# Performance work log

Hardware: AMD Instinct MI355X
Metric: run time of the kernel (lower is better)

## Reference

```python
import jax, jax.numpy as jnp
import numpy as np

N, E, IN_F, EDGE_F, HID, S = 200000, 600000, 28, 4, 128, 20000
NUM_LAYERS = 4
L = NUM_LAYERS - 1
BN_EPS = 1e-5


def setup_inputs() -> dict:
    key = jax.random.key(0)
    ks = jax.random.split(key, 20)
    p = lambda k, shape: (jax.random.normal(k, shape, dtype=jnp.float32) * 0.1)
    return {
        'x': jax.random.normal(ks[0], (N, IN_F), dtype=jnp.float32),
        'edge_index': jax.random.randint(ks[1], (2, E), 0, N),
        'edge_attr': jax.random.normal(ks[2], (E, EDGE_F), dtype=jnp.float32),
        'edge_weight': jax.random.uniform(ks[3], (E,), dtype=jnp.float32),
        'node_mask': (jax.random.uniform(ks[4], (N,)) > 0.5).astype(jnp.float32),
        'subgraphs2nodes': jax.random.randint(ks[5], (N,), 0, S),
        # layer-1 params (in_features -> hidden)
        'be1_W1': p(ks[6], (EDGE_F, IN_F)), 'be1_b1': jnp.zeros((IN_F,), jnp.float32),
        'be1_W2': p(ks[7], (IN_F, IN_F)), 'be1_b2': jnp.zeros((IN_F,), jnp.float32),
        'm1_W1': p(ks[8], (IN_F, HID)), 'm1_b1': jnp.zeros((HID,), jnp.float32),
        'm1_W2': p(ks[9], (HID, HID)), 'm1_b2': jnp.zeros((HID,), jnp.float32),
        'bn1_g': jnp.ones((HID,), jnp.float32), 'bn1_b': jnp.zeros((HID,), jnp.float32),
        'eps1': jnp.zeros((), jnp.float32),
        # layers 2..NUM_LAYERS, stacked (hidden -> hidden)
        'beW1': p(ks[10], (L, EDGE_F, HID)), 'beb1': jnp.zeros((L, HID), jnp.float32),
        'beW2': p(ks[11], (L, HID, HID)), 'beb2': jnp.zeros((L, HID), jnp.float32),
        'mW1': p(ks[12], (L, HID, HID)), 'mb1': jnp.zeros((L, HID), jnp.float32),
        'mW2': p(ks[13], (L, HID, HID)), 'mb2': jnp.zeros((L, HID), jnp.float32),
        'bng': jnp.ones((L, HID), jnp.float32), 'bnb': jnp.zeros((L, HID), jnp.float32),
        'eps': jnp.zeros((L,), jnp.float32),
    }


def _mlp2(h, W1, b1, W2, b2):
    # Linear -> ReLU -> Linear
    return jnp.dot(jax.nn.relu(jnp.dot(h, W1) + b1), W2) + b2


def _gine(x, src, dst, edge_attr, edge_weight, eps,
          beW1, beb1, beW2, beb2, W1, b1, W2, b2, g, beta):
    # bond encoder on edge features
    e = _mlp2(edge_attr, beW1, beb1, beW2, beb2)            # [E, d]
    # message: relu(x_j + e_ij) * w_ij, aggregated at dst via scatter-add
    m = jax.nn.relu(x[src] + e) * edge_weight[:, None]      # [E, d]
    aggr = jax.ops.segment_sum(m, dst, num_segments=N)      # [N, d]
    h = (1.0 + eps) * x + aggr
    # node MLP: Linear,ReLU,Linear,BN(train mode),ReLU
    h = _mlp2(h, W1, b1, W2, b2)
    mu = jnp.mean(h, axis=0)
    var = jnp.mean((h - mu) ** 2, axis=0)
    h = (h - mu) * jax.lax.rsqrt(var + BN_EPS) * g + beta
    return jax.nn.relu(h)


def reference(x, edge_index, edge_attr, edge_weight, node_mask, subgraphs2nodes,
              be1_W1, be1_b1, be1_W2, be1_b2, m1_W1, m1_b1, m1_W2, m1_b2,
              bn1_g, bn1_b, eps1,
              beW1, beb1, beW2, beb2, mW1, mb1, mW2, mb2, bng, bnb, eps):
    src, dst = edge_index[0], edge_index[1]
    h = _gine(x, src, dst, edge_attr, edge_weight, eps1,
              be1_W1, be1_b1, be1_W2, be1_b2,
              m1_W1, m1_b1, m1_W2, m1_b2, bn1_g, bn1_b)
    for i in range(L):
        h_new = _gine(h, src, dst, edge_attr, edge_weight, eps[i],
                      beW1[i], beb1[i], beW2[i], beb2[i],
                      mW1[i], mb1[i], mW2[i], mb2[i], bng[i], bnb[i])
        h = h + h_new  # residual
    # float node_mask branch + global_add_pool over subgraphs2nodes
    h = h * node_mask[:, None]
    return jax.ops.segment_sum(h, subgraphs2nodes, num_segments=S)  # [S, HID]
```

## Files before the change

kernel.cpp:

```cpp
#include <hip/hip_runtime.h>
#include <hip/hip_bf16.h>


#define BNEPS 1e-5f
#define LDA 136
#define SCAN_NB 240

typedef __attribute__((ext_vector_type(8))) short bf16x8;
typedef __attribute__((ext_vector_type(8))) unsigned short u16x8;
typedef __attribute__((ext_vector_type(4))) float f32x4;

__device__ inline short f2bf(float f) {
    __hip_bfloat16 h = __float2bfloat16(f);
    return *reinterpret_cast<short*>(&h);
}
__device__ inline unsigned short f2bfu(float f) {
    __hip_bfloat16 h = __float2bfloat16(f);
    return *reinterpret_cast<unsigned short*>(&h);
}
__device__ inline float bf2f(unsigned short u) {
    union { unsigned int i; float f; } v; v.i = ((unsigned int)u) << 16; return v.f;
}


__global__ __launch_bounds__(256) void k_prep(
    const float* __restrict__ m1W2, const float* __restrict__ beW2,
    const float* __restrict__ mW1, const float* __restrict__ mW2,
    const float* __restrict__ m1W1, const float* __restrict__ be1W2,
    short* __restrict__ out, short* __restrict__ out1, short* __restrict__ out28)
{
    __shared__ float tileS[64][65];
    int b = blockIdx.x;
    if (b == 40) {
        for (int i = threadIdx.x; i < 4096; i += 256) {
            int j = i & 7, sub = (i >> 3) & 63, nt = i >> 9;
            int quad = sub >> 4, l15 = sub & 15;
            int n = nt * 16 + l15, k = quad * 8 + j;
            out1[i] = (k < 28) ? f2bf(m1W1[(size_t)k * 128 + n]) : (short)0;
        }
        return;
    }
    if (b == 41) {
        for (int i = threadIdx.x; i < 1024; i += 256) {
            int j = i & 7, lane = (i >> 3) & 63, nt = i >> 9;
            int quad = lane >> 4, l15 = lane & 15;
            int n = nt * 16 + l15, k = quad * 8 + j;
            out28[i] = (n < 28 && k < 28) ? f2bf(be1W2[(size_t)k * 28 + n]) : (short)0;
        }
        return;
    }
    int mat = b >> 2, t = b & 3;
    const float* Wsrc;
    if (mat == 0) Wsrc = m1W2;
    else {
        int l = (mat - 1) / 3, which = (mat - 1) % 3;
        Wsrc = (which == 0) ? beW2 + (size_t)l * 16384
             : (which == 1) ? mW1 + (size_t)l * 16384
             :                mW2 + (size_t)l * 16384;
    }
    short* dst = out + (size_t)mat * 16384;
    int tr = (t >> 1) * 64, tc = (t & 1) * 64;
    for (int i = threadIdx.x; i < 4096; i += 256) {
        int r = i >> 6, c = i & 63;
        tileS[r][c] = Wsrc[(size_t)(tr + r) * 128 + (tc + c)];
    }
    __syncthreads();
    for (int i = threadIdx.x; i < 4096; i += 256) {
        int kl = i & 63, nl = i >> 6;
        int n = tc + nl, k = tr + kl;
        int fo = (((n >> 4) * 4 + (k >> 5)) * 64 + (((k >> 3) & 3) * 16 + (n & 15))) * 8 + (k & 7);
        dst[fo] = f2bf(tileS[kl][nl]);
    }
}

__global__ __launch_bounds__(256) void k_prepx(
    const float* __restrict__ x, unsigned short* __restrict__ xbf, int N)
{
    int total = N * 32;
    for (int i = blockIdx.x * 256 + threadIdx.x; i < total; i += gridDim.x * 256) {
        int n = i >> 5, c = i & 31;
        xbf[i] = (c < 28) ? f2bfu(x[(size_t)n * 28 + c]) : (unsigned short)0;
    }
}

__global__ __launch_bounds__(256) void k_count(
    const int* __restrict__ ei, int* __restrict__ counts, int E)
{
    for (int e = blockIdx.x * 256 + threadIdx.x; e < E; e += gridDim.x * 256)
        atomicAdd(&counts[ei[E + e]], 1);
}

__global__ __launch_bounds__(256) void k_count2(
    const int* __restrict__ s2n, const float* __restrict__ mask,
    int* __restrict__ counts2, int N)
{
    for (int n = blockIdx.x * 256 + threadIdx.x; n < N; n += gridDim.x * 256)
        if (mask[n] != 0.f) atomicAdd(&counts2[s2n[n]], 1);
}

__global__ __launch_bounds__(256) void k_scanA(
    const int* __restrict__ counts, int* __restrict__ bsum, int N, int seg)
{
    __shared__ int red[256];
    int b = blockIdx.x;
    int lo = b * seg, hi = min(lo + seg, N);
    int s = 0;
    for (int i = lo + threadIdx.x; i < hi; i += 256) s += counts[i];
    red[threadIdx.x] = s;
    __syncthreads();
    for (int d = 128; d > 0; d >>= 1) {
        if (threadIdx.x < d) red[threadIdx.x] += red[threadIdx.x + d];
        __syncthreads();
    }
    if (threadIdx.x == 0) bsum[b] = red[0];
}

__global__ __launch_bounds__(256) void k_scanB(
    int* __restrict__ bsum, int nb, int* __restrict__ offs, int N)
{
    __shared__ int sh[256];
    int v = (threadIdx.x < nb) ? bsum[threadIdx.x] : 0;
    sh[threadIdx.x] = v;
    __syncthreads();
    for (int d = 1; d < 256; d <<= 1) {
        int t = (threadIdx.x >= d) ? sh[threadIdx.x - d] : 0;
        __syncthreads();
        sh[threadIdx.x] += t;
        __syncthreads();
    }
    if (threadIdx.x < nb) bsum[threadIdx.x] = sh[threadIdx.x] - v;
    if (threadIdx.x == 0) offs[N] = sh[255];
}

__global__ __launch_bounds__(256) void k_scanC(
    const int* __restrict__ counts, const int* __restrict__ bsum,
    int* __restrict__ offs, int* __restrict__ cursor, int N, int seg)
{
    __shared__ int sh[256];
    int b = blockIdx.x;
    int lo = b * seg, hi = min(lo + seg, N);
    int base = bsum[b];
    for (int t0 = lo; t0 < hi; t0 += 256) {
        int i = t0 + threadIdx.x;
        int v = (i < hi) ? counts[i] : 0;
        sh[threadIdx.x] = v;
        __syncthreads();
        for (int d = 1; d < 256; d <<= 1) {
            int t = (threadIdx.x >= d) ? sh[threadIdx.x - d] : 0;
            __syncthreads();
            sh[threadIdx.x] += t;
            __syncthreads();
        }
        int excl = base + sh[threadIdx.x] - v;
        if (i < hi) { offs[i] = excl; cursor[i] = excl; }
        int tileTotal = sh[255];
        __syncthreads();
        base += tileTotal;
    }
}

__global__ __launch_bounds__(256) void k_scatter(
    const int* __restrict__ ei, const float* __restrict__ ew,
    const float4* __restrict__ ea4,
    int* __restrict__ cursor, int2* __restrict__ pmeta,
    float4* __restrict__ pea4, int E)
{
    for (int e = blockIdx.x * 256 + threadIdx.x; e < E; e += gridDim.x * 256) {
        int d = ei[E + e];
        int pos = atomicAdd(&cursor[d], 1);
        pmeta[pos] = make_int2(ei[e], __float_as_int(ew[e]));
        pea4[pos] = ea4[e];
    }
}

__global__ __launch_bounds__(256) void k_scatter2(
    const int* __restrict__ s2n, const float* __restrict__ mask,
    int* __restrict__ cursor2, int* __restrict__ perm2, int N)
{
    for (int n = blockIdx.x * 256 + threadIdx.x; n < N; n += gridDim.x * 256)
        if (mask[n] != 0.f) {
            int pos = atomicAdd(&cursor2[s2n[n]], 1);
            perm2[pos] = n;
        }
}

__global__ __launch_bounds__(256, 3) void k_emsg(
    const float4* __restrict__ pea4,
    const float* __restrict__ W1, const float* __restrict__ b1,
    const short* __restrict__ W2f, const float* __restrict__ b2,
    unsigned short* __restrict__ emsg, const int* __restrict__ offs,
    int n0, int n1)
{
    __shared__ short As[64 * LDA];
    __shared__ short Bs[16384];
    int e0 = offs[n0], e1 = offs[n1];
    int tid = threadIdx.x;
    int w = tid >> 6, lane = tid & 63;
    int l15 = lane & 15, quad = lane >> 4;
    int rb = w * 16;
    for (int i = tid; i < 2048; i += 256)
        *(bf16x8*)&Bs[i * 8] = *(const bf16x8*)&W2f[i * 8];
    int c2 = lane * 2;
    float w1a[4], w1b[4];
    #pragma unroll
    for (int a = 0; a < 4; ++a) { w1a[a] = W1[a * 128 + c2]; w1b[a] = W1[a * 128 + c2 + 1]; }
    float b1a = b1[c2], b1b = b1[c2 + 1];
    float b2r[8];
    #pragma unroll
    for (int nt = 0; nt < 8; ++nt) b2r[nt] = b2[nt * 16 + l15];
    __syncthreads();

    const float* peaf = (const float*)pea4;
    int numTiles = (e1 - e0 + 63) >> 6;
    for (int tile = blockIdx.x; tile < numTiles; tile += gridDim.x) {
        int base = e0 + tile * 64;
        int eidx = base + rb + (lane >> 2);
        float v = (eidx < e1) ? peaf[(size_t)(base + rb) * 4 + lane] : 0.f;
        #pragma unroll
        for (int e = 0; e < 16; ++e) {
            float a0v = __shfl(v, e * 4 + 0);
            float a1v = __shfl(v, e * 4 + 1);
            float a2v = __shfl(v, e * 4 + 2);
            float a3v = __shfl(v, e * 4 + 3);
            float t0 = fmaf(a0v, w1a[0], fmaf(a1v, w1a[1], fmaf(a2v, w1a[2], fmaf(a3v, w1a[3], b1a))));
            float t1 = fmaf(a0v, w1b[0], fmaf(a1v, w1b[1], fmaf(a2v, w1b[2], fmaf(a3v, w1b[3], b1b))));
            unsigned int pk = ((unsigned int)f2bfu(fmaxf(t1, 0.f)) << 16) | f2bfu(fmaxf(t0, 0.f));
            *(unsigned int*)&As[(rb + e) * LDA + c2] = pk;
        }
        f32x4 acc[8];
        #pragma unroll
        for (int nt = 0; nt < 8; ++nt) acc[nt] = (f32x4){0.f, 0.f, 0.f, 0.f};
        #pragma unroll
        for (int kt = 0; kt < 4; ++kt) {
            bf16x8 af = *(bf16x8*)&As[(rb + l15) * LDA + kt * 32 + quad * 8];
            #pragma unroll
            for (int nt = 0; nt < 8; ++nt) {
                bf16x8 bf = *(const bf16x8*)&Bs[((nt * 4 + kt) * 64 + lane) * 8];
                acc[nt] = __builtin_amdgcn_mfma_f32_16x16x32_bf16(af, bf, acc[nt], 0, 0, 0);
            }
        }
        #pragma unroll
        for (int nt = 0; nt < 8; ++nt) {
            #pragma unroll
            for (int r = 0; r < 4; ++r)
                As[(rb + quad * 4 + r) * LDA + nt * 16 + l15] = f2bf(acc[nt][r] + b2r[nt]);
        }
        #pragma unroll
        for (int it = 0; it < 4; ++it) {
            int arow = rb + it * 4 + quad;
            int gr = base + arow;
            if (gr < e1)
                *(bf16x8*)&emsg[(size_t)(gr - e0) * 128 + l15 * 8] = *(bf16x8*)&As[arow * LDA + l15 * 8];
        }
    }
}

__global__ __launch_bounds__(256, 4) void k_emsg28_mm(
    const float4* __restrict__ pea4,
    const float* __restrict__ W1, const float* __restrict__ b1,
    const short* __restrict__ W2f28,
    const float* __restrict__ b2,
    unsigned short* __restrict__ emsg28, int E)
{
    __shared__ short As[64 * 40];
    int tid = threadIdx.x;
    int w = tid >> 6, lane = tid & 63;
    int l15 = lane & 15, quad = lane >> 4;
    int rb = w * 16;
    bf16x8 B0 = *(const bf16x8*)&W2f28[(size_t)lane * 8];
    bf16x8 B1 = *(const bf16x8*)&W2f28[(size_t)(64 + lane) * 8];
    int c2 = l15 * 2;
    bool act = (c2 < 28);
    float w1a[4], w1b[4], b1a, b1b;
    #pragma unroll
    for (int a = 0; a < 4; ++a) {
        w1a[a] = act ? W1[a * 28 + c2] : 0.f;
        w1b[a] = act ? W1[a * 28 + c2 + 1] : 0.f;
    }
    b1a = act ? b1[c2] : 0.f;
    b1b = act ? b1[c2 + 1] : 0.f;
    float b2r0 = b2[l15];
    float b2r1 = (l15 < 12) ? b2[16 + l15] : 0.f;

    const float* peaf = (const float*)pea4;
    int numTiles = (E + 63) >> 6;
    for (int tile = blockIdx.x; tile < numTiles; tile += gridDim.x) {
        int base = tile * 64;
        int eidx = base + rb + (lane >> 2);
        float v = (eidx < E) ? peaf[(size_t)(base + rb) * 4 + lane] : 0.f;
        #pragma unroll
        for (int e = 0; e < 16; ++e) {
            float a0v = __shfl(v, e * 4 + 0);
            float a1v = __shfl(v, e * 4 + 1);
            float a2v = __shfl(v, e * 4 + 2);
            float a3v = __shfl(v, e * 4 + 3);
            float t0 = fmaf(a0v, w1a[0], fmaf(a1v, w1a[1], fmaf(a2v, w1a[2], fmaf(a3v, w1a[3], b1a))));
            float t1 = fmaf(a0v, w1b[0], fmaf(a1v, w1b[1], fmaf(a2v, w1b[2], fmaf(a3v, w1b[3], b1b))));
            unsigned int pk = ((unsigned int)f2bfu(fmaxf(t1, 0.f)) << 16) | f2bfu(fmaxf(t0, 0.f));
            if (quad == (e & 3))
                *(unsigned int*)&As[(rb + e) * 40 + c2] = pk;
        }
        f32x4 acc0 = (f32x4){0.f, 0.f, 0.f, 0.f};
        f32x4 acc1 = (f32x4){0.f, 0.f, 0.f, 0.f};
        bf16x8 af = *(bf16x8*)&As[(rb + l15) * 40 + quad * 8];
        acc0 = __builtin_amdgcn_mfma_f32_16x16x32_bf16(af, B0, acc0, 0, 0, 0);
        acc1 = __builtin_amdgcn_mfma_f32_16x16x32_bf16(af, B1, acc1, 0, 0, 0);
        #pragma unroll
        for (int r = 0; r < 4; ++r) {
            As[(rb + quad * 4 + r) * 40 + l15] = f2bf(acc0[r] + b2r0);
            As[(rb + quad * 4 + r) * 40 + 16 + l15] = f2bf(acc1[r] + b2r1);
        }
        #pragma unroll
        for (int it = 0; it < 4; ++it) {
            int arow = rb + it * 4 + quad;
            int gr = base + arow;
            if (gr < E && l15 < 14)
                *(ushort2*)&emsg28[(size_t)gr * 28 + c2] = *(ushort2*)&As[arow * 40 + c2];
        }
    }
}

__global__ __launch_bounds__(256) void k_gather(
    const unsigned short* __restrict__ h, const int* __restrict__ offs,
    const int2* __restrict__ pmeta, const unsigned short* __restrict__ emsg,
    unsigned short* __restrict__ a0,
    const float* __restrict__ epsp, int epsIdx,
    int n0, int n1)
{
    int grp = threadIdx.x >> 5, lane = threadIdx.x & 31;
    int n = n0 + blockIdx.x * 8 + grp;
    if (n >= n1) return;
    int e0 = offs[n0];
    int k0 = offs[n], k1 = offs[n + 1];
    float s = 1.0f + epsp[epsIdx];
    ushort4 hv0 = *(const ushort4*)&h[(size_t)n * 128 + lane * 4];
    float m0 = s * bf2f(hv0.x), m1 = s * bf2f(hv0.y);
    float m2 = s * bf2f(hv0.z), m3 = s * bf2f(hv0.w);
    int2 mtA, mtB;
    ushort4 evA, hvA, evB, hvB;
    if (k0 < k1) {
        mtA = pmeta[k0];
        evA = *(const ushort4*)&emsg[(size_t)(k0 - e0) * 128 + lane * 4];
        hvA = *(const ushort4*)&h[(size_t)mtA.x * 128 + lane * 4];
    }
    if (k0 + 1 < k1) {
        mtB = pmeta[k0 + 1];
        evB = *(const ushort4*)&emsg[(size_t)(k0 + 1 - e0) * 128 + lane * 4];
        hvB = *(const ushort4*)&h[(size_t)mtB.x * 128 + lane * 4];
    }
    for (int k = k0; k < k1; ++k) {
        float w = __int_as_float(mtA.y);
        m0 += fmaxf(bf2f(hvA.x) + bf2f(evA.x), 0.f) * w;
        m1 += fmaxf(bf2f(hvA.y) + bf2f(evA.y), 0.f) * w;
        m2 += fmaxf(bf2f(hvA.z) + bf2f(evA.z), 0.f) * w;
        m3 += fmaxf(bf2f(hvA.w) + bf2f(evA.w), 0.f) * w;
        mtA = mtB; evA = evB; hvA = hvB;
        if (k + 2 < k1) {
            mtB = pmeta[k + 2];
            evB = *(const ushort4*)&emsg[(size_t)(k + 2 - e0) * 128 + lane * 4];
            hvB = *(const ushort4*)&h[(size_t)mtB.x * 128 + lane * 4];
        }
    }
    ushort4 o;
    o.x = f2bfu(m0); o.y = f2bfu(m1); o.z = f2bfu(m2); o.w = f2bfu(m3);
    *(ushort4*)&a0[(size_t)n * 128 + lane * 4] = o;
}

__global__ __launch_bounds__(256) void k_gather28(
    const float* __restrict__ x, const unsigned short* __restrict__ xbf,
    const int* __restrict__ offs,
    const int2* __restrict__ pmeta, const unsigned short* __restrict__ emsg28,
    const float* __restrict__ eps1, float* __restrict__ u28, int N)
{
    int grp = threadIdx.x >> 5, lane = threadIdx.x & 31;
    int n = blockIdx.x * 8 + grp;
    if (n >= N || lane >= 28) return;
    float s = 1.0f + eps1[0];
    int k0 = offs[n], k1 = offs[n + 1];
    float m = 0.f;
    int2 mtA, mtB;
    unsigned short eA = 0, xA = 0, eB = 0, xB = 0;
    if (k0 < k1) {
        mtA = pmeta[k0];
        eA = emsg28[(size_t)k0 * 28 + lane];
        xA = xbf[(size_t)mtA.x * 32 + lane];
    }
    if (k0 + 1 < k1) {
        mtB = pmeta[k0 + 1];
        eB = emsg28[(size_t)(k0 + 1) * 28 + lane];
        xB = xbf[(size_t)mtB.x * 32 + lane];
    }
    for (int k = k0; k < k1; ++k) {
        float w = __int_as_float(mtA.y);
        m += fmaxf(bf2f(xA) + bf2f(eA), 0.f) * w;
        mtA = mtB; eA = eB; xA = xB;
        if (k + 2 < k1) {
            mtB = pmeta[k + 2];
            eB = emsg28[(size_t)(k + 2) * 28 + lane];
            xB = xbf[(size_t)mtB.x * 32 + lane];
        }
    }
    u28[(size_t)n * 28 + lane] = fmaf(s, x[(size_t)n * 28 + lane], m);
}

__global__ __launch_bounds__(1024, 4) void k_mlp(
    const unsigned short* __restrict__ src, const short* __restrict__ W1f,
    const float* __restrict__ b1, const short* __restrict__ W2f,
    const float* __restrict__ b2, unsigned short* __restrict__ dst,
    float* __restrict__ stats, int N)
{
    __shared__ short Bs1[16384];
    __shared__ short Bs2[16384];
    __shared__ short As[16 * 16 * LDA];
    __shared__ float sstat[256];
    int tid = threadIdx.x;
    for (int i = tid; i < 2048; i += 1024) {
        *(bf16x8*)&Bs1[i * 8] = *(const bf16x8*)&W1f[i * 8];
        *(bf16x8*)&Bs2[i * 8] = *(const bf16x8*)&W2f[i * 8];
    }
    if (tid < 256) sstat[tid] = 0.f;
    int w = tid >> 6, lane = tid & 63;
    int l15 = lane & 15, quad = lane >> 4;
    short* myAs = &As[w * 16 * LDA];
    float b1r[8], b2r[8], lsum[8], lsq[8];
    #pragma unroll
    for (int nt = 0; nt < 8; ++nt) {
        b1r[nt] = b1[nt * 16 + l15]; b2r[nt] = b2[nt * 16 + l15];
        lsum[nt] = 0.f; lsq[nt] = 0.f;
    }
    __syncthreads();

    int numTiles = (N + 255) >> 8;
    for (int tile = blockIdx.x; tile < numTiles; tile += gridDim.x) {
        int rowbase = tile * 256 + w * 16;
        int arow = rowbase + l15;
        const unsigned short* srow = src + (size_t)arow * 128;
        f32x4 acc[8];
        #pragma unroll
        for (int nt = 0; nt < 8; ++nt) acc[nt] = (f32x4){0.f, 0.f, 0.f, 0.f};
        #pragma unroll
        for (int kt = 0; kt < 4; ++kt) {
            bf16x8 af = (arow < N) ? *(const bf16x8*)&srow[kt * 32 + quad * 8]
                                   : (bf16x8){0, 0, 0, 0, 0, 0, 0, 0};
            #pragma unroll
            for (int nt = 0; nt < 8; ++nt) {
                bf16x8 bf = *(const bf16x8*)&Bs1[((nt * 4 + kt) * 64 + lane) * 8];
                acc[nt] = __builtin_amdgcn_mfma_f32_16x16x32_bf16(af, bf, acc[nt], 0, 0, 0);
            }
        }
        #pragma unroll
        for (int nt = 0; nt < 8; ++nt)
            #pragma unroll
            for (int r = 0; r < 4; ++r)
                myAs[(quad * 4 + r) * LDA + nt * 16 + l15] =
                    f2bf(fmaxf(acc[nt][r] + b1r[nt], 0.f));
        #pragma unroll
        for (int nt = 0; nt < 8; ++nt) acc[nt] = (f32x4){0.f, 0.f, 0.f, 0.f};
        #pragma unroll
        for (int kt = 0; kt < 4; ++kt) {
            bf16x8 af = *(bf16x8*)&myAs[l15 * LDA + kt * 32 + quad * 8];
            #pragma unroll
            for (int nt = 0; nt < 8; ++nt) {
                bf16x8 bf = *(const bf16x8*)&Bs2[((nt * 4 + kt) * 64 + lane) * 8];
                acc[nt] = __builtin_amdgcn_mfma_f32_16x16x32_bf16(af, bf, acc[nt], 0, 0, 0);
            }
        }
        #pragma unroll
        for (int nt = 0; nt < 8; ++nt) {
            int row0 = rowbase + quad * 4;
            #pragma unroll
            for (int r = 0; r < 4; ++r) {
                float z = acc[nt][r] + b2r[nt];
                if (row0 + r < N) { lsum[nt] += z; lsq[nt] = fmaf(z, z, lsq[nt]); }
                myAs[(quad * 4 + r) * LDA + nt * 16 + l15] = f2bf(z);
            }
        }
        #pragma unroll
        for (int s = 0; s < 4; ++s) {
            int i = lane + s * 64;
            int lrow = i >> 4, c8 = i & 15;
            int rr = rowbase + lrow;
            if (rr < N)
                *(bf16x8*)&dst[(size_t)rr * 128 + c8 * 8] = *(bf16x8*)&myAs[lrow * LDA + c8 * 8];
        }
    }
    #pragma unroll
    for (int nt = 0; nt < 8; ++nt) {
        atomicAdd(&sstat[nt * 16 + l15], lsum[nt]);
        atomicAdd(&sstat[128 + nt * 16 + l15], lsq[nt]);
    }
    __syncthreads();
    if (tid < 256) atomicAdd(&stats[tid], sstat[tid]);
}

__global__ __launch_bounds__(1024, 4) void k_mlp1(
    const float* __restrict__ u28, const short* __restrict__ W1f,
    const float* __restrict__ b1, const short* __restrict__ W2f,
    const float* __restrict__ b2, unsigned short* __restrict__ dst,
    float* __restrict__ stats, int N)
{
    __shared__ short Bs1[4096];
    __shared__ short Bs2[16384];
    __shared__ short As[16 * 16 * LDA];
    __shared__ float sstat[256];
    int tid = threadIdx.x;
    if (tid < 512)
        *(bf16x8*)&Bs1[tid * 8] = *(const bf16x8*)&W1f[tid * 8];
    for (int i = tid; i < 2048; i += 1024)
        *(bf16x8*)&Bs2[i * 8] = *(const bf16x8*)&W2f[i * 8];
    if (tid < 256) sstat[tid] = 0.f;
    int w = tid >> 6, lane = tid & 63;
    int l15 = lane & 15, quad = lane >> 4;
    short* myAs = &As[w * 16 * LDA];
    float b1r[8], b2r[8], lsum[8], lsq[8];
    #pragma unroll
    for (int nt = 0; nt < 8; ++nt) {
        b1r[nt] = b1[nt * 16 + l15]; b2r[nt] = b2[nt * 16 + l15];
        lsum[nt] = 0.f; lsq[nt] = 0.f;
    }
    __syncthreads();

    int numTiles = (N + 255) >> 8;
    for (int tile = blockIdx.x; tile < numTiles; tile += gridDim.x) {
        int rowbase = tile * 256 + w * 16;
        int arow = rowbase + l15;
        const float* urow = u28 + (size_t)arow * 28;
        float4 fa = make_float4(0.f, 0.f, 0.f, 0.f);
        float4 fb = make_float4(0.f, 0.f, 0.f, 0.f);
        if (arow < N) {
            fa = *(const float4*)&urow[quad * 8];
            if (quad < 3) fb = *(const float4*)&urow[quad * 8 + 4];
        }
        bf16x8 af1;
        af1[0] = f2bf(fa.x); af1[1] = f2bf(fa.y); af1[2] = f2bf(fa.z); af1[3] = f2bf(fa.w);
        af1[4] = f2bf(fb.x); af1[5] = f2bf(fb.y); af1[6] = f2bf(fb.z); af1[7] = f2bf(fb.w);
        f32x4 acc[8];
        #pragma unroll
        for (int nt = 0; nt < 8; ++nt) acc[nt] = (f32x4){0.f, 0.f, 0.f, 0.f};
        #pragma unroll
        for (int nt = 0; nt < 8; ++nt) {
            bf16x8 bf = *(const bf16x8*)&Bs1[(nt * 64 + lane) * 8];
            acc[nt] = __builtin_amdgcn_mfma_f32_16x16x32_bf16(af1, bf, acc[nt], 0, 0, 0);
        }
        #pragma unroll
        for (int nt = 0; nt < 8; ++nt)
            #pragma unroll
            for (int r = 0; r < 4; ++r)
                myAs[(quad * 4 + r) * LDA + nt * 16 + l15] =
                    f2bf(fmaxf(acc[nt][r] + b1r[nt], 0.f));
        #pragma unroll
        for (int nt = 0; nt < 8; ++nt) acc[nt] = (f32x4){0.f, 0.f, 0.f, 0.f};
        #pragma unroll
        for (int kt = 0; kt < 4; ++kt) {
            bf16x8 af = *(bf16x8*)&myAs[l15 * LDA + kt * 32 + quad * 8];
            #pragma unroll
            for (int nt = 0; nt < 8; ++nt) {
                bf16x8 bf = *(const bf16x8*)&Bs2[((nt * 4 + kt) * 64 + lane) * 8];
                acc[nt] = __builtin_amdgcn_mfma_f32_16x16x32_bf16(af, bf, acc[nt], 0, 0, 0);
            }
        }
        #pragma unroll
        for (int nt = 0; nt < 8; ++nt) {
            int row0 = rowbase + quad * 4;
            #pragma unroll
            for (int r = 0; r < 4; ++r) {
                float z = acc[nt][r] + b2r[nt];
                if (row0 + r < N) { lsum[nt] += z; lsq[nt] = fmaf(z, z, lsq[nt]); }
                myAs[(quad * 4 + r) * LDA + nt * 16 + l15] = f2bf(z);
            }
        }
        #pragma unroll
        for (int s = 0; s < 4; ++s) {
            int i = lane + s * 64;
            int lrow = i >> 4, c8 = i & 15;
            int rr = rowbase + lrow;
            if (rr < N)
                *(bf16x8*)&dst[(size_t)rr * 128 + c8 * 8] = *(bf16x8*)&myAs[lrow * LDA + c8 * 8];
        }
    }
    #pragma unroll
    for (int nt = 0; nt < 8; ++nt) {
        atomicAdd(&sstat[nt * 16 + l15], lsum[nt]);
        atomicAdd(&sstat[128 + nt * 16 + l15], lsq[nt]);
    }
    __syncthreads();
    if (tid < 256) atomicAdd(&stats[tid], sstat[tid]);
}

__global__ __launch_bounds__(128) void k_stats(
    const float* __restrict__ stats, const float* __restrict__ g,
    const float* __restrict__ b, float* __restrict__ ss, float invN)
{
    int j = threadIdx.x;
    float mu  = stats[j] * invN;
    float var = fmaf(stats[128 + j], invN, -mu * mu);
    float sc  = rsqrtf(fmaxf(var, 0.f) + BNEPS) * g[j];
    ss[j] = sc;
    ss[128 + j] = fmaf(-mu, sc, b[j]);
}

__global__ __launch_bounds__(256) void k_bn(
    const unsigned short* __restrict__ z, const float* __restrict__ ss,
    unsigned short* __restrict__ h, int residual, int N)
{
    int idx8 = blockIdx.x * 256 + threadIdx.x;
    int stride = gridDim.x * 256;
    int c0 = (idx8 & 15) * 8;
    float scl[8], sht[8];
    #pragma unroll
    for (int r = 0; r < 8; ++r) { scl[r] = ss[c0 + r]; sht[r] = ss[128 + c0 + r]; }
    int total8 = N * 16;
    for (; idx8 < total8; idx8 += stride) {
        int n = idx8 >> 4;
        u16x8 z8 = *(const u16x8*)&z[(size_t)n * 128 + c0];
        float hn[8];
        #pragma unroll
        for (int r = 0; r < 8; ++r)
            hn[r] = fmaxf(fmaf(bf2f(z8[r]), scl[r], sht[r]), 0.f);
        if (residual) {
            u16x8 h8 = *(const u16x8*)&h[(size_t)n * 128 + c0];
            #pragma unroll
            for (int r = 0; r < 8; ++r) hn[r] += bf2f(h8[r]);
        }
        u16x8 o;
        #pragma unroll
        for (int r = 0; r < 8; ++r) o[r] = f2bfu(hn[r]);
        *(u16x8*)&h[(size_t)n * 128 + c0] = o;
    }
}

__global__ __launch_bounds__(256) void k_poolbn(
    const unsigned short* __restrict__ z, const unsigned short* __restrict__ hprev,
    const float* __restrict__ ss, const int* __restrict__ offs2,
    const int* __restrict__ perm2, float* __restrict__ out, int S)
{
    int w = threadIdx.x >> 6, lane = threadIdx.x & 63;
    int s = blockIdx.x * 4 + w;
    if (s >= S) return;
    int c0 = lane * 2;
    float scl0 = ss[c0], scl1 = ss[c0 + 1];
    float sht0 = ss[128 + c0], sht1 = ss[128 + c0 + 1];
    int k0 = offs2[s], k1 = offs2[s + 1];
    float a0 = 0.f, a1 = 0.f;
    for (int k = k0; k < k1; ++k) {
        int n = perm2[k];
        ushort2 zv = *(const ushort2*)&z[(size_t)n * 128 + c0];
        ushort2 hv = *(const ushort2*)&hprev[(size_t)n * 128 + c0];
        a0 += fmaxf(fmaf(bf2f(zv.x), scl0, sht0), 0.f) + bf2f(hv.x);
        a1 += fmaxf(fmaf(bf2f(zv.y), scl1, sht1), 0.f) + bf2f(hv.y);
    }
    *(float2*)&out[(size_t)s * 128 + c0] = make_float2(a0, a1);
}

extern "C" void kernel_launch(void* const* d_in, const int* in_sizes, int n_in,
                              void* d_out, int out_size, void* d_ws, size_t ws_size,
                              hipStream_t stream) {
    const float* x    = (const float*)d_in[0];
    const int*   ei   = (const int*)d_in[1];
    const float* ea   = (const float*)d_in[2];
    const float* ew   = (const float*)d_in[3];
    const float* mask = (const float*)d_in[4];
    const int*   s2n  = (const int*)d_in[5];
    const float* be1W1 = (const float*)d_in[6];
    const float* be1b1 = (const float*)d_in[7];
    const float* be1W2 = (const float*)d_in[8];
    const float* be1b2 = (const float*)d_in[9];
    const float* m1W1  = (const float*)d_in[10];
    const float* m1b1  = (const float*)d_in[11];
    const float* m1W2  = (const float*)d_in[12];
    const float* m1b2  = (const float*)d_in[13];
    const float* bn1g  = (const float*)d_in[14];
    const float* bn1b  = (const float*)d_in[15];
    const float* eps1  = (const float*)d_in[16];
    const float* beW1  = (const float*)d_in[17];
    const float* beb1  = (const float*)d_in[18];
    const float* beW2  = (const float*)d_in[19];
    const float* beb2  = (const float*)d_in[20];
    const float* mW1   = (const float*)d_in[21];
    const float* mb1   = (const float*)d_in[22];
    const float* mW2   = (const float*)d_in[23];
    const float* mb2   = (const float*)d_in[24];
    const float* bng   = (const float*)d_in[25];
    const float* bnb   = (const float*)d_in[26];
    const float* epsL  = (const float*)d_in[27];

    const int N = in_sizes[0] / 28;
    const int E = in_sizes[1] / 2;
    const int S = out_size / 128;
    const float invN = 1.0f / (float)N;
    const int NS = N / 2;
    const int EMC = E / 2 + 8192;

    auto al16 = [](size_t v) { return (v + 15) & ~(size_t)15; };
    char* ws = (char*)d_ws;
    size_t offH      = 0;
    size_t offA0     = al16(offH + (size_t)N * 256);
    size_t offEm     = al16(offA0 + (size_t)N * 256);
    size_t emBytes   = (size_t)EMC * 256;
    if ((size_t)E * 56 > emBytes) emBytes = (size_t)E * 56;
    size_t offStats  = al16(offEm + emBytes);
    size_t offSS     = al16(offStats + 4096);
    size_t offWts    = al16(offSS + 1024);
    size_t offCounts = al16(offWts + 10 * 16384 * 2 + 4096 * 2 + 1024 * 2);
    size_t offOffs   = al16(offCounts + (size_t)N * 4);
    size_t offCursor = al16(offOffs + (size_t)(N + 1) * 4);
    size_t offPmeta  = al16(offCursor + (size_t)N * 4);
    size_t offPea    = al16(offPmeta + (size_t)E * 8);
    size_t offBsum   = al16(offPea + (size_t)E * 16);
    size_t offCnt2   = al16(offBsum + SCAN_NB * 4);
    size_t offOffs2  = al16(offCnt2 + (size_t)S * 4);
    size_t offCur2   = al16(offOffs2 + (size_t)(S + 1) * 4);
    size_t offPerm2  = al16(offCur2 + (size_t)S * 4);
    size_t need      = offPerm2 + (size_t)N * 4;
    if (ws_size < need) return;

    unsigned short* h    = (unsigned short*)(ws + offH);
    unsigned short* a0   = (unsigned short*)(ws + offA0);
    unsigned short* emsg = (unsigned short*)(ws + offEm);
    float* u28    = (float*)(ws + offA0);
    unsigned short* xbf = (unsigned short*)(ws + offA0 + 26214400);
    float* stats  = (float*)(ws + offStats);
    float* ssbuf  = (float*)(ws + offSS);
    short* wts    = (short*)(ws + offWts);
    short* w1p    = wts + 10 * 16384;
    short* w2p28  = w1p + 4096;
    int*   counts = (int*)(ws + offCounts);
    int*   offs   = (int*)(ws + offOffs);
    int*   cursor = (int*)(ws + offCursor);
    int2*  pmeta  = (int2*)(ws + offPmeta);
    float4* pea4  = (float4*)(ws + offPea);
    int*   bsum   = (int*)(ws + offBsum);
    int*   cnt2   = (int*)(ws + offCnt2);
    int*   offs2  = (int*)(ws + offOffs2);
    int*   cur2   = (int*)(ws + offCur2);
    int*   perm2  = (int*)(ws + offPerm2);
    const float4* ea4 = (const float4*)ea;

    hipMemsetAsync(stats, 0, 4 * 256 * sizeof(float), stream);
    hipMemsetAsync(counts, 0, (size_t)N * sizeof(int), stream);
    hipMemsetAsync(cnt2, 0, (size_t)S * sizeof(int), stream);

    k_prep<<<42, 256, 0, stream>>>(m1W2, beW2, mW1, mW2, m1W1, be1W2, wts, w1p, w2p28);
    k_prepx<<<512, 256, 0, stream>>>(x, xbf, N);

    const int seg = (N + SCAN_NB - 1) / SCAN_NB;
    k_count<<<1024, 256, 0, stream>>>(ei, counts, E);
    k_scanA<<<SCAN_NB, 256, 0, stream>>>(counts, bsum, N, seg);
    k_scanB<<<1, 256, 0, stream>>>(bsum, SCAN_NB, offs, N);
    k_scanC<<<SCAN_NB, 256, 0, stream>>>(counts, bsum, offs, cursor, N, seg);
    k_scatter<<<1024, 256, 0, stream>>>(ei, ew, ea4, cursor, pmeta, pea4, E);

    const int seg2 = (S + SCAN_NB - 1) / SCAN_NB;
    k_count2<<<512, 256, 0, stream>>>(s2n, mask, cnt2, N);
    k_scanA<<<SCAN_NB, 256, 0, stream>>>(cnt2, bsum, S, seg2);
    k_scanB<<<1, 256, 0, stream>>>(bsum, SCAN_NB, offs2, S);
    k_scanC<<<SCAN_NB, 256, 0, stream>>>(cnt2, bsum, offs2, cur2, S, seg2);
    k_scatter2<<<512, 256, 0, stream>>>(s2n, mask, cur2, perm2, N);

    auto wt_be = [&](int l) { return wts + (size_t)(1 + 3 * l + 0) * 16384; };
    auto wt_m1 = [&](int l) { return wts + (size_t)(1 + 3 * l + 1) * 16384; };
    auto wt_m2 = [&](int l) { return wts + (size_t)(1 + 3 * l + 2) * 16384; };

    k_emsg28_mm<<<2048, 256, 0, stream>>>(pea4, be1W1, be1b1, w2p28, be1b2, emsg, E);
    k_gather28<<<(N + 7) / 8, 256, 0, stream>>>(x, xbf, offs, pmeta, emsg, eps1, u28, N);
    k_mlp1<<<256, 1024, 0, stream>>>(u28, w1p, m1b1, wts , m1b2, h, stats, N);
    k_stats<<<1, 128, 0, stream>>>(stats, bn1g, bn1b, ssbuf, invN);
    k_bn<<<2048, 256, 0, stream>>>(h, ssbuf, h, 0, N);

    for (int l = 0; l < 3; ++l) {
        for (int c = 0; c < 2; ++c) {
            int n0 = (c == 0) ? 0 : NS;
            int n1 = (c == 0) ? NS : N;
            k_emsg<<<2048, 256, 0, stream>>>(pea4,
                beW1 + (size_t)l * 512, beb1 + (size_t)l * 128,
                wt_be(l), beb2 + (size_t)l * 128, emsg, offs, n0, n1);
            k_gather<<<(n1 - n0 + 7) / 8, 256, 0, stream>>>(h, offs, pmeta, emsg, a0,
                epsL, l, n0, n1);
        }
        k_mlp<<<256, 1024, 0, stream>>>(a0, wt_m1(l), mb1 + (size_t)l * 128,
                                        wt_m2(l), mb2 + (size_t)l * 128, a0,
                                        stats + 256 * (l + 1), N);
        k_stats<<<1, 128, 0, stream>>>(stats + 256 * (l + 1),
            bng + (size_t)l * 128, bnb + (size_t)l * 128, ssbuf, invN);
        if (l < 2) {
            k_bn<<<2048, 256, 0, stream>>>(a0, ssbuf, h, 1, N);
        }
    }

    k_poolbn<<<(S + 3) / 4, 256, 0, stream>>>(a0, h, ssbuf, offs2, perm2,
                                              (float*)d_out, S);
}
```

Baseline: 1.056 ms.

## Fuse edge-message MLP with neighbor gather via per-block LDS atomic aggregation

Replaces the separate edge-encoder kernel, which wrote bf16 edge embeddings to global memory, and the per-node gather kernel with one fused kernel per layer. Each block owns a contiguous range of destination nodes, computes the edge MLP with MFMA for that node range's CSR-sorted edges, gathers source features, and accumulates messages into shared-memory fp32 accumulators with LDS atomics. This removes the global round-trip of the E×128 message tensor and the bf16 x copy, at the cost of LDS atomics, a larger LDS footprint with lower occupancy, a new pdst array, and load imbalance from varying edge counts per block.

Result: slower. 2.227 ms (+110.8%).

```diff
diff --git a/kernel.cpp b/kernel.cpp
--- a/kernel.cpp
+++ b/kernel.cpp
@@ -5,6 +5,8 @@
 #define BNEPS 1e-5f
 #define LDA 136
 #define SCAN_NB 240
+#define NPB 48
+#define NPB28 64
 
 typedef __attribute__((ext_vector_type(8))) short bf16x8;
 typedef __attribute__((ext_vector_type(8))) unsigned short u16x8;
@@ -70,16 +72,6 @@
         int n = tc + nl, k = tr + kl;
         int fo = (((n >> 4) * 4 + (k >> 5)) * 64 + (((k >> 3) & 3) * 16 + (n & 15))) * 8 + (k & 7);
         dst[fo] = f2bf(tileS[kl][nl]);
-    }
-}
-
-__global__ __launch_bounds__(256) void k_prepx(
-    const float* __restrict__ x, unsigned short* __restrict__ xbf, int N)
-{
-    int total = N * 32;
-    for (int i = blockIdx.x * 256 + threadIdx.x; i < total; i += gridDim.x * 256) {
-        int n = i >> 5, c = i & 31;
-        xbf[i] = (c < 28) ? f2bfu(x[(size_t)n * 28 + c]) : (unsigned short)0;
     }
 }
 
@@ -163,12 +155,13 @@
     const int* __restrict__ ei, const float* __restrict__ ew,
     const float4* __restrict__ ea4,
     int* __restrict__ cursor, int2* __restrict__ pmeta,
-    float4* __restrict__ pea4, int E)
+    int* __restrict__ pdst, float4* __restrict__ pea4, int E)
 {
     for (int e = blockIdx.x * 256 + threadIdx.x; e < E; e += gridDim.x * 256) {
         int d = ei[E + e];
         int pos = atomicAdd(&cursor[d], 1);
         pmeta[pos] = make_int2(ei[e], __float_as_int(ew[e]));
+        pdst[pos] = d;
         pea4[pos] = ea4[e];
     }
 }
@@ -184,22 +177,28 @@
         }
 }
 
-__global__ __launch_bounds__(256, 3) void k_emsg(
+__global__ __launch_bounds__(256, 2) void k_eg(
     const float4* __restrict__ pea4,
     const float* __restrict__ W1, const float* __restrict__ b1,
     const short* __restrict__ W2f, const float* __restrict__ b2,
-    unsigned short* __restrict__ emsg, const int* __restrict__ offs,
-    int n0, int n1)
+    const int2* __restrict__ pmeta, const int* __restrict__ pdst,
+    const unsigned short* __restrict__ h, const int* __restrict__ offs,
+    const float* __restrict__ epsp, int epsIdx,
+    unsigned short* __restrict__ a0, int N)
 {
     __shared__ short As[64 * LDA];
     __shared__ short Bs[16384];
-    int e0 = offs[n0], e1 = offs[n1];
+    __shared__ float acc[NPB * 128];
     int tid = threadIdx.x;
+    int nb0 = blockIdx.x * NPB;
+    int nb1 = min(nb0 + NPB, N);
+    int eb0 = offs[nb0], eb1 = offs[nb1];
     int w = tid >> 6, lane = tid & 63;
     int l15 = lane & 15, quad = lane >> 4;
     int rb = w * 16;
     for (int i = tid; i < 2048; i += 256)
         *(bf16x8*)&Bs[i * 8] = *(const bf16x8*)&W2f[i * 8];
+    for (int i = tid; i < NPB * 128; i += 256) acc[i] = 0.f;
     int c2 = lane * 2;
     float w1a[4], w1b[4];
     #pragma unroll
@@ -211,11 +210,22 @@
     __syncthreads();
 
     const float* peaf = (const float*)pea4;
-    int numTiles = (e1 - e0 + 63) >> 6;
-    for (int tile = blockIdx.x; tile < numTiles; tile += gridDim.x) {
-        int base = e0 + tile * 64;
-        int eidx = base + rb + (lane >> 2);
-        float v = (eidx < e1) ? peaf[(size_t)(base + rb) * 4 + lane] : 0.f;
+    for (int ebase = eb0 + w * 16; ebase < eb1; ebase += 64) {
+        float v = (ebase + (lane >> 2) < eb1) ? peaf[(size_t)ebase * 4 + lane] : 0.f;
+        int srcv = 0, wbits = 0, dstv = nb0;
+        if (lane < 16) {
+            int e = ebase + lane;
+            if (e < eb1) {
+                int2 mt = pmeta[e];
+                srcv = mt.x; wbits = mt.y; dstv = pdst[e];
+            }
+        }
+        unsigned int hsv[16];
+        #pragma unroll
+        for (int e = 0; e < 16; ++e) {
+            int se = __shfl(srcv, e);
+            hsv[e] = *(const unsigned int*)&h[(size_t)se * 128 + c2];
+        }
         #pragma unroll
         for (int e = 0; e < 16; ++e) {
             float a0v = __shfl(v, e * 4 + 0);
@@ -227,67 +237,107 @@
             unsigned int pk = ((unsigned int)f2bfu(fmaxf(t1, 0.f)) << 16) | f2bfu(fmaxf(t0, 0.f));
             *(unsigned int*)&As[(rb + e) * LDA + c2] = pk;
         }
-        f32x4 acc[8];
-        #pragma unroll
-        for (int nt = 0; nt < 8; ++nt) acc[nt] = (f32x4){0.f, 0.f, 0.f, 0.f};
+        f32x4 zacc[8];
+        #pragma unroll
+        for (int nt = 0; nt < 8; ++nt) zacc[nt] = (f32x4){0.f, 0.f, 0.f, 0.f};
         #pragma unroll
         for (int kt = 0; kt < 4; ++kt) {
             bf16x8 af = *(bf16x8*)&As[(rb + l15) * LDA + kt * 32 + quad * 8];
             #pragma unroll
             for (int nt = 0; nt < 8; ++nt) {
                 bf16x8 bf = *(const bf16x8*)&Bs[((nt * 4 + kt) * 64 + lane) * 8];
-                acc[nt] = __builtin_amdgcn_mfma_f32_16x16x32_bf16(af, bf, acc[nt], 0, 0, 0);
+                zacc[nt] = __builtin_amdgcn_mfma_f32_16x16x32_bf16(af, bf, zacc[nt], 0, 0, 0);
             }
         }
         #pragma unroll
         for (int nt = 0; nt < 8; ++nt) {
             #pragma unroll
             for (int r = 0; r < 4; ++r)
-                As[(rb + quad * 4 + r) * LDA + nt * 16 + l15] = f2bf(acc[nt][r] + b2r[nt]);
-        }
-        #pragma unroll
-        for (int it = 0; it < 4; ++it) {
-            int arow = rb + it * 4 + quad;
-            int gr = base + arow;
-            if (gr < e1)
-                *(bf16x8*)&emsg[(size_t)(gr - e0) * 128 + l15 * 8] = *(bf16x8*)&As[arow * LDA + l15 * 8];
-        }
-    }
-}
-
-__global__ __launch_bounds__(256, 4) void k_emsg28_mm(
+                As[(rb + quad * 4 + r) * LDA + nt * 16 + l15] = f2bf(zacc[nt][r] + b2r[nt]);
+        }
+        #pragma unroll
+        for (int e = 0; e < 16; ++e) {
+            float we = __int_as_float(__shfl(wbits, e));
+            int de = __shfl(dstv, e);
+            unsigned int zp = *(unsigned int*)&As[(rb + e) * LDA + c2];
+            unsigned int hp = hsv[e];
+            float m0 = fmaxf(bf2f((unsigned short)(hp & 0xffff)) + bf2f((unsigned short)(zp & 0xffff)), 0.f) * we;
+            float m1 = fmaxf(bf2f((unsigned short)(hp >> 16)) + bf2f((unsigned short)(zp >> 16)), 0.f) * we;
+            float* ap = &acc[(de - nb0) * 128 + c2];
+            atomicAdd(ap, m0);
+            atomicAdd(ap + 1, m1);
+        }
+    }
+    __syncthreads();
+    float s = 1.0f + epsp[epsIdx];
+    int items = (nb1 - nb0) * 16;
+    for (int i = tid; i < items; i += 256) {
+        int node = i >> 4, c8 = (i & 15) * 8;
+        int n = nb0 + node;
+        u16x8 hv = *(const u16x8*)&h[(size_t)n * 128 + c8];
+        u16x8 o;
+        #pragma unroll
+        for (int r = 0; r < 8; ++r)
+            o[r] = f2bfu(fmaf(s, bf2f(hv[r]), acc[node * 128 + c8 + r]));
+        *(u16x8*)&a0[(size_t)n * 128 + c8] = o;
+    }
+}
+
+__global__ __launch_bounds__(256, 4) void k_eg28(
     const float4* __restrict__ pea4,
     const float* __restrict__ W1, const float* __restrict__ b1,
-    const short* __restrict__ W2f28,
-    const float* __restrict__ b2,
-    unsigned short* __restrict__ emsg28, int E)
+    const short* __restrict__ W2f28, const float* __restrict__ b2,
+    const int2* __restrict__ pmeta, const int* __restrict__ pdst,
+    const float* __restrict__ x, const int* __restrict__ offs,
+    const float* __restrict__ eps1, float* __restrict__ u28, int N)
 {
     __shared__ short As[64 * 40];
+    __shared__ float acc[NPB28 * 28];
     int tid = threadIdx.x;
+    int nb0 = blockIdx.x * NPB28;
+    int nb1 = min(nb0 + NPB28, N);
+    int eb0 = offs[nb0], eb1 = offs[nb1];
     int w = tid >> 6, lane = tid & 63;
     int l15 = lane & 15, quad = lane >> 4;
     int rb = w * 16;
+    for (int i = tid; i < NPB28 * 28; i += 256) acc[i] = 0.f;
     bf16x8 B0 = *(const bf16x8*)&W2f28[(size_t)lane * 8];
     bf16x8 B1 = *(const bf16x8*)&W2f28[(size_t)(64 + lane) * 8];
-    int c2 = l15 * 2;
-    bool act = (c2 < 28);
+    int c2w = l15 * 2;
+    bool actw = (c2w < 28);
     float w1a[4], w1b[4], b1a, b1b;
     #pragma unroll
     for (int a = 0; a < 4; ++a) {
-        w1a[a] = act ? W1[a * 28 + c2] : 0.f;
-        w1b[a] = act ? W1[a * 28 + c2 + 1] : 0.f;
-    }
-    b1a = act ? b1[c2] : 0.f;
-    b1b = act ? b1[c2 + 1] : 0.f;
+        w1a[a] = actw ? W1[a * 28 + c2w] : 0.f;
+        w1b[a] = actw ? W1[a * 28 + c2w + 1] : 0.f;
+    }
+    b1a = actw ? b1[c2w] : 0.f;
+    b1b = actw ? b1[c2w + 1] : 0.f;
     float b2r0 = b2[l15];
     float b2r1 = (l15 < 12) ? b2[16 + l15] : 0.f;
+    int c2m = lane * 2;
+    bool actm = (c2m < 28);
+    __syncthreads();
 
     const float* peaf = (const float*)pea4;
-    int numTiles = (E + 63) >> 6;
-    for (int tile = blockIdx.x; tile < numTiles; tile += gridDim.x) {
-        int base = tile * 64;
-        int eidx = base + rb + (lane >> 2);
-        float v = (eidx < E) ? peaf[(size_t)(base + rb) * 4 + lane] : 0.f;
+    for (int ebase = eb0 + w * 16; ebase < eb1; ebase += 64) {
+        float v = (ebase + (lane >> 2) < eb1) ? peaf[(size_t)ebase * 4 + lane] : 0.f;
+        int srcv = 0, wbits = 0, dstv = nb0;
+        if (lane < 16) {
+            int e = ebase + lane;
+            if (e < eb1) {
+                int2 mt = pmeta[e];
+                srcv = mt.x; wbits = mt.y; dstv = pdst[e];
+            }
+        }
+        float xs0[16], xs1[16];
+        #pragma unroll
+        for (int e = 0; e < 16; ++e) {
+            int se = __shfl(srcv, e);
+            float2 xv = make_float2(0.f, 0.f);
+            if (actm) xv = *(const float2*)&x[(size_t)se * 28 + c2m];
+            xs0[e] = xv.x; xs1[e] = xv.y;
+        }
         #pragma unroll
         for (int e = 0; e < 16; ++e) {
             float a0v = __shfl(v, e * 4 + 0);
@@ -298,7 +348,7 @@
             float t1 = fmaf(a0v, w1b[0], fmaf(a1v, w1b[1], fmaf(a2v, w1b[2], fmaf(a3v, w1b[3], b1b))));
             unsigned int pk = ((unsigned int)f2bfu(fmaxf(t1, 0.f)) << 16) | f2bfu(fmaxf(t0, 0.f));
             if (quad == (e & 3))
-                *(unsigned int*)&As[(rb + e) * 40 + c2] = pk;
+                *(unsigned int*)&As[(rb + e) * 40 + c2w] = pk;
         }
         f32x4 acc0 = (f32x4){0.f, 0.f, 0.f, 0.f};
         f32x4 acc1 = (f32x4){0.f, 0.f, 0.f, 0.f};
@@ -311,96 +361,27 @@
             As[(rb + quad * 4 + r) * 40 + 16 + l15] = f2bf(acc1[r] + b2r1);
         }
         #pragma unroll
-        for (int it = 0; it < 4; ++it) {
-            int arow = rb + it * 4 + quad;
-            int gr = base + arow;
-            if (gr < E && l15 < 14)
-                *(ushort2*)&emsg28[(size_t)gr * 28 + c2] = *(ushort2*)&As[arow * 40 + c2];
-        }
-    }
-}
-
-__global__ __launch_bounds__(256) void k_gather(
-    const unsigned short* __restrict__ h, const int* __restrict__ offs,
-    const int2* __restrict__ pmeta, const unsigned short* __restrict__ emsg,
-    unsigned short* __restrict__ a0,
-    const float* __restrict__ epsp, int epsIdx,
-    int n0, int n1)
-{
-    int grp = threadIdx.x >> 5, lane = threadIdx.x & 31;
-    int n = n0 + blockIdx.x * 8 + grp;
-    if (n >= n1) return;
-    int e0 = offs[n0];
-    int k0 = offs[n], k1 = offs[n + 1];
-    float s = 1.0f + epsp[epsIdx];
-    ushort4 hv0 = *(const ushort4*)&h[(size_t)n * 128 + lane * 4];
-    float m0 = s * bf2f(hv0.x), m1 = s * bf2f(hv0.y);
-    float m2 = s * bf2f(hv0.z), m3 = s * bf2f(hv0.w);
-    int2 mtA, mtB;
-    ushort4 evA, hvA, evB, hvB;
-    if (k0 < k1) {
-        mtA = pmeta[k0];
-        evA = *(const ushort4*)&emsg[(size_t)(k0 - e0) * 128 + lane * 4];
-        hvA = *(const ushort4*)&h[(size_t)mtA.x * 128 + lane * 4];
-    }
-    if (k0 + 1 < k1) {
-        mtB = pmeta[k0 + 1];
-        evB = *(const ushort4*)&emsg[(size_t)(k0 + 1 - e0) * 128 + lane * 4];
-        hvB = *(const ushort4*)&h[(size_t)mtB.x * 128 + lane * 4];
-    }
-    for (int k = k0; k < k1; ++k) {
-        float w = __int_as_float(mtA.y);
-        m0 += fmaxf(bf2f(hvA.x) + bf2f(evA.x), 0.f) * w;
-        m1 += fmaxf(bf2f(hvA.y) + bf2f(evA.y), 0.f) * w;
-        m2 += fmaxf(bf2f(hvA.z) + bf2f(evA.z), 0.f) * w;
-        m3 += fmaxf(bf2f(hvA.w) + bf2f(evA.w), 0.f) * w;
-        mtA = mtB; evA = evB; hvA = hvB;
-        if (k + 2 < k1) {
-            mtB = pmeta[k + 2];
-            evB = *(const ushort4*)&emsg[(size_t)(k + 2 - e0) * 128 + lane * 4];
-            hvB = *(const ushort4*)&h[(size_t)mtB.x * 128 + lane * 4];
-        }
-    }
-    ushort4 o;
-    o.x = f2bfu(m0); o.y = f2bfu(m1); o.z = f2bfu(m2); o.w = f2bfu(m3);
-    *(ushort4*)&a0[(size_t)n * 128 + lane * 4] = o;
-}
-
-__global__ __launch_bounds__(256) void k_gather28(
-    const float* __restrict__ x, const unsigned short* __restrict__ xbf,
-    const int* __restrict__ offs,
-    const int2* __restrict__ pmeta, const unsigned short* __restrict__ emsg28,
-    const float* __restrict__ eps1, float* __restrict__ u28, int N)
-{
-    int grp = threadIdx.x >> 5, lane = threadIdx.x & 31;
-    int n = blockIdx.x * 8 + grp;
-    if (n >= N || lane >= 28) return;
+        for (int e = 0; e < 16; ++e) {
+            float we = __int_as_float(__shfl(wbits, e));
+            int de = __shfl(dstv, e);
+            if (actm) {
+                unsigned int zp = *(unsigned int*)&As[(rb + e) * 40 + c2m];
+                float m0 = fmaxf(xs0[e] + bf2f((unsigned short)(zp & 0xffff)), 0.f) * we;
+                float m1 = fmaxf(xs1[e] + bf2f((unsigned short)(zp >> 16)), 0.f) * we;
+                float* ap = &acc[(de - nb0) * 28 + c2m];
+                atomicAdd(ap, m0);
+                atomicAdd(ap + 1, m1);
+            }
+        }
+    }
+    __syncthreads();
     float s = 1.0f + eps1[0];
-    int k0 = offs[n], k1 = offs[n + 1];
-    float m = 0.f;
-    int2 mtA, mtB;
-    unsigned short eA = 0, xA = 0, eB = 0, xB = 0;
-    if (k0 < k1) {
-        mtA = pmeta[k0];
-        eA = emsg28[(size_t)k0 * 28 + lane];
-        xA = xbf[(size_t)mtA.x * 32 + lane];
-    }
-    if (k0 + 1 < k1) {
-        mtB = pmeta[k0 + 1];
-        eB = emsg28[(size_t)(k0 + 1) * 28 + lane];
-        xB = xbf[(size_t)mtB.x * 32 + lane];
-    }
-    for (int k = k0; k < k1; ++k) {
-        float w = __int_as_float(mtA.y);
-        m += fmaxf(bf2f(xA) + bf2f(eA), 0.f) * w;
-        mtA = mtB; eA = eB; xA = xB;
-        if (k + 2 < k1) {
-            mtB = pmeta[k + 2];
-            eB = emsg28[(size_t)(k + 2) * 28 + lane];
-            xB = xbf[(size_t)mtB.x * 32 + lane];
-        }
-    }
-    u28[(size_t)n * 28 + lane] = fmaf(s, x[(size_t)n * 28 + lane], m);
+    int items = (nb1 - nb0) * 28;
+    for (int i = tid; i < items; i += 256) {
+        int node = i / 28, c = i - node * 28;
+        int n = nb0 + node;
+        u28[(size_t)n * 28 + c] = fmaf(s, x[(size_t)n * 28 + c], acc[node * 28 + c]);
+    }
 }
 
 __global__ __launch_bounds__(1024, 4) void k_mlp(
@@ -688,7 +669,6 @@
     const int E = in_sizes[1] / 2;
     const int S = out_size / 128;
     const float invN = 1.0f / (float)N;
-    const int NS = N / 2;
     const int EMC = E / 2 + 8192;
 
     auto al16 = [](size_t v) { return (v + 15) & ~(size_t)15; };
@@ -716,9 +696,8 @@
 
     unsigned short* h    = (unsigned short*)(ws + offH);
     unsigned short* a0   = (unsigned short*)(ws + offA0);
-    unsigned short* emsg = (unsigned short*)(ws + offEm);
     float* u28    = (float*)(ws + offA0);
-    unsigned short* xbf = (unsigned short*)(ws + offA0 + 26214400);
+    int*   pdst   = (int*)(ws + offEm);
     float* stats  = (float*)(ws + offStats);
     float* ssbuf  = (float*)(ws + offSS);
     short* wts    = (short*)(ws + offWts);
@@ -741,14 +720,13 @@
     hipMemsetAsync(cnt2, 0, (size_t)S * sizeof(int), stream);
 
     k_prep<<<42, 256, 0, stream>>>(m1W2, beW2, mW1, mW2, m1W1, be1W2, wts, w1p, w2p28);
-    k_prepx<<<512, 256, 0, stream>>>(x, xbf, N);
 
     const int seg = (N + SCAN_NB - 1) / SCAN_NB;
     k_count<<<1024, 256, 0, stream>>>(ei, counts, E);
     k_scanA<<<SCAN_NB, 256, 0, stream>>>(counts, bsum, N, seg);
     k_scanB<<<1, 256, 0, stream>>>(bsum, SCAN_NB, offs, N);
     k_scanC<<<SCAN_NB, 256, 0, stream>>>(counts, bsum, offs, cursor, N, seg);
-    k_scatter<<<1024, 256, 0, stream>>>(ei, ew, ea4, cursor, pmeta, pea4, E);
+    k_scatter<<<1024, 256, 0, stream>>>(ei, ew, ea4, cursor, pmeta, pdst, pea4, E);
 
     const int seg2 = (S + SCAN_NB - 1) / SCAN_NB;
     k_count2<<<512, 256, 0, stream>>>(s2n, mask, cnt2, N);
@@ -761,22 +739,17 @@
     auto wt_m1 = [&](int l) { return wts + (size_t)(1 + 3 * l + 1) * 16384; };
     auto wt_m2 = [&](int l) { return wts + (size_t)(1 + 3 * l + 2) * 16384; };
 
-    k_emsg28_mm<<<2048, 256, 0, stream>>>(pea4, be1W1, be1b1, w2p28, be1b2, emsg, E);
-    k_gather28<<<(N + 7) / 8, 256, 0, stream>>>(x, xbf, offs, pmeta, emsg, eps1, u28, N);
+    k_eg28<<<(N + NPB28 - 1) / NPB28, 256, 0, stream>>>(
+        pea4, be1W1, be1b1, w2p28, be1b2, pmeta, pdst, x, offs, eps1, u28, N);
     k_mlp1<<<256, 1024, 0, stream>>>(u28, w1p, m1b1, wts , m1b2, h, stats, N);
     k_stats<<<1, 128, 0, stream>>>(stats, bn1g, bn1b, ssbuf, invN);
     k_bn<<<2048, 256, 0, stream>>>(h, ssbuf, h, 0, N);
 
     for (int l = 0; l < 3; ++l) {
-        for (int c = 0; c < 2; ++c) {
-            int n0 = (c == 0) ? 0 : NS;
-            int n1 = (c == 0) ? NS : N;
-            k_emsg<<<2048, 256, 0, stream>>>(pea4,
-                beW1 + (size_t)l * 512, beb1 + (size_t)l * 128,
-                wt_be(l), beb2 + (size_t)l * 128, emsg, offs, n0, n1);
-            k_gather<<<(n1 - n0 + 7) / 8, 256, 0, stream>>>(h, offs, pmeta, emsg, a0,
-                epsL, l, n0, n1);
-        }
+        k_eg<<<(N + NPB - 1) / NPB, 256, 0, stream>>>(
+            pea4, beW1 + (size_t)l * 512, beb1 + (size_t)l * 128,
+            wt_be(l), beb2 + (size_t)l * 128, pmeta, pdst, h, offs,
+            epsL, l, a0, N);
         k_mlp<<<256, 1024, 0, stream>>>(a0, wt_m1(l), mb1 + (size_t)l * 128,
                                         wt_m2(l), mb2 + (size_t)l * 128, a0,
                                         stats + 256 * (l + 1), N);
```
